# Optimization experiments

Hardware: AMD Instinct MI355X
Metric: run time of the kernel (lower is better)

The kernel has to match this reference:

```python
import jax, jax.numpy as jnp
import numpy as np

S, B, IN = 16384, 1, 8
H = 2048          # hidden_dim
TAG = 2048        # tagset_size
QCNN_DIMS = [(8, 16), (16, 16), (16, 12), (12, 4), (4, 4), (4, 4), (4, 1)]


def _linear_params(key, fan_in, fan_out):
    kw, kb = jax.random.split(key)
    bound = 1.0 / np.sqrt(fan_in)
    w = jax.random.uniform(kw, (fan_in, fan_out), jnp.float32, -bound, bound)
    b = jax.random.uniform(kb, (fan_out,), jnp.float32, -bound, bound)
    return w, b


def setup_inputs() -> dict:
    key = jax.random.key(0)
    keys = jax.random.split(key, 16)
    inp = {"sentence": jax.random.normal(keys[0], (S, B, IN), jnp.float32)}
    names = [("fm", 0), ("c1", 1), ("p1", 2), ("c2", 3), ("p2", 4), ("c3", 5), ("h", 6)]
    for i, (nm, di) in enumerate(names):
        w, b = _linear_params(keys[1 + i], *QCNN_DIMS[di])
        inp[f"{nm}_w"], inp[f"{nm}_b"] = w, b
    for i, g in enumerate(["f", "i", "u", "o"]):
        w, b = _linear_params(keys[8 + i], 1 + H, H)
        inp[f"w{g}"], inp[f"b{g}"] = w, b
    wt, bt = _linear_params(keys[12], H, TAG)
    inp["wt"], inp["bt"] = wt, bt
    return inp


def reference(sentence, fm_w, fm_b, c1_w, c1_b, p1_w, p1_b, c2_w, c2_b,
              p2_w, p2_b, c3_w, c3_b, h_w, h_b,
              wf, bf, wi, bi, wu, bu, wo, bo, wt, bt):
    seq_len, batch, _ = sentence.shape
    t = jnp.tanh
    # ---- ClassicalQCNN: dense MLP chain on flattened tokens ----
    x = sentence.reshape(seq_len * batch, -1)
    x = t(x @ fm_w + fm_b)
    x = t(x @ c1_w + c1_b)
    x = t(x @ p1_w + p1_b)
    x = t(x @ c2_w + c2_b)
    x = t(x @ p2_w + p2_b)
    x = t(x @ c3_w + c3_b)
    x = jax.nn.sigmoid(x @ h_w + h_b)          # (S*B, 1)
    seq = x.reshape(seq_len, batch, 1)

    # ---- ClassicalQLSTM: fuse 4 gate linears into one GEMM per step ----
    w_gates = jnp.concatenate([wf, wi, wu, wo], axis=1)   # (1+H, 4H)
    b_gates = jnp.concatenate([bf, bi, bu, bo])           # (4H,)
    hidden = wf.shape[1]

    def step(carry, x_t):
        hx, cx = carry
        combined = jnp.concatenate([x_t, hx], axis=1)     # (B, 1+H)
        gates = combined @ w_gates + b_gates              # (B, 4H)
        f, i, g, o = jnp.split(gates, 4, axis=1)
        cx = jax.nn.sigmoid(f) * cx + jax.nn.sigmoid(i) * jnp.tanh(g)
        hx = jax.nn.sigmoid(o) * jnp.tanh(cx)
        return (hx, cx), hx

    init = (jnp.zeros((batch, hidden), sentence.dtype),
            jnp.zeros((batch, hidden), sentence.dtype))
    _, lstm_out = jax.lax.scan(step, init, seq)           # (S, B, H)

    logits = lstm_out.reshape(seq_len, -1) @ wt + bt      # batch==1 => (S, TAG)
    return jax.nn.log_softmax(logits, axis=1)
```

## Files before the change

kernel.cpp:

```cpp
#include <hip/hip_runtime.h>
#include <stdint.h>

#define S_LEN 16384
#define HID 2048
#define NPAIR 1024

typedef _Float16 h2v __attribute__((ext_vector_type(2)));

__device__ __forceinline__ float dot2f(uint32_t a, uint32_t b, float c) {
#if __has_builtin(__builtin_amdgcn_fdot2)
  return __builtin_amdgcn_fdot2(__builtin_bit_cast(h2v, a), __builtin_bit_cast(h2v, b), c, false);
#else
  h2v ha = __builtin_bit_cast(h2v, a), hb = __builtin_bit_cast(h2v, b);
  return c + (float)ha[0] * (float)hb[0] + (float)ha[1] * (float)hb[1];
#endif
}

__device__ __forceinline__ uint32_t packh2(float a, float b) {
  h2v h; h[0] = (_Float16)a; h[1] = (_Float16)b;
  return __builtin_bit_cast(uint32_t, h);
}

__device__ __forceinline__ float fsig(float x) { return 1.0f / (1.0f + __expf(-x)); }
__device__ __forceinline__ float ftanh(float x) { return 2.0f / (1.0f + __expf(-2.0f * x)) - 1.0f; }

__device__ __forceinline__ float wave_reduce_add(float x) {
#define DPP_STEP(ctrl)                                                                   \
  {                                                                                      \
    int t_ = __builtin_amdgcn_update_dpp(0, __builtin_bit_cast(int, x), ctrl, 0xf, 0xf, true); \
    x += __builtin_bit_cast(float, t_);                                                  \
  }
  DPP_STEP(0x111)
  DPP_STEP(0x112)
  DPP_STEP(0x114)
  DPP_STEP(0x118)
  DPP_STEP(0x142)
  DPP_STEP(0x143)
#undef DPP_STEP
  return x;
}

__global__ __launch_bounds__(256) void qcnn_kernel(
    const float* __restrict__ sent,
    const float* __restrict__ fm_w, const float* __restrict__ fm_b,
    const float* __restrict__ c1w, const float* __restrict__ c1b,
    const float* __restrict__ p1w, const float* __restrict__ p1b,
    const float* __restrict__ c2w, const float* __restrict__ c2b,
    const float* __restrict__ p2w, const float* __restrict__ p2b,
    const float* __restrict__ c3w, const float* __restrict__ c3b,
    const float* __restrict__ hw, const float* __restrict__ hb,
    float* __restrict__ seq, unsigned long long* __restrict__ hbuf) {
  __shared__ float w[720];
  const int tid = threadIdx.x;
  const float* srcs[14] = {fm_w, fm_b, c1w, c1b, p1w, p1b, c2w, c2b, p2w, p2b, c3w, c3b, hw, hb};
  const int offs[14] = {0, 128, 144, 400, 416, 608, 620, 668, 672, 688, 692, 708, 712, 716};
  const int cnts[14] = {128, 16, 256, 16, 192, 12, 48, 4, 16, 4, 16, 4, 4, 1};
  for (int a = 0; a < 14; ++a)
    for (int i = tid; i < cnts[a]; i += 256) w[offs[a] + i] = srcs[a][i];
  if (blockIdx.x == 0) {
    for (int p = tid; p < NPAIR; p += 256) {
      hbuf[p] = 0ull;
      hbuf[NPAIR + p] = 0x7FFFFFFFull << 32;
    }
  }
  __syncthreads();
  const int t = blockIdx.x * 256 + tid;
  float x[8];
#pragma unroll
  for (int i = 0; i < 8; ++i) x[i] = sent[t * 8 + i];
  float a0[16], a1[16], a2[12], a3[4], a4[4], a5[4];
#pragma unroll
  for (int o = 0; o < 16; ++o) {
    float s = w[128 + o];
#pragma unroll
    for (int i = 0; i < 8; ++i) s += x[i] * w[i * 16 + o];
    a0[o] = ftanh(s);
  }
#pragma unroll
  for (int o = 0; o < 16; ++o) {
    float s = w[400 + o];
#pragma unroll
    for (int i = 0; i < 16; ++i) s += a0[i] * w[144 + i * 16 + o];
    a1[o] = ftanh(s);
  }
#pragma unroll
  for (int o = 0; o < 12; ++o) {
    float s = w[608 + o];
#pragma unroll
    for (int i = 0; i < 16; ++i) s += a1[i] * w[416 + i * 12 + o];
    a2[o] = ftanh(s);
  }
#pragma unroll
  for (int o = 0; o < 4; ++o) {
    float s = w[668 + o];
#pragma unroll
    for (int i = 0; i < 12; ++i) s += a2[i] * w[620 + i * 4 + o];
    a3[o] = ftanh(s);
  }
#pragma unroll
  for (int o = 0; o < 4; ++o) {
    float s = w[688 + o];
#pragma unroll
    for (int i = 0; i < 4; ++i) s += a3[i] * w[672 + i * 4 + o];
    a4[o] = ftanh(s);
  }
#pragma unroll
  for (int o = 0; o < 4; ++o) {
    float s = w[708 + o];
#pragma unroll
    for (int i = 0; i < 4; ++i) s += a4[i] * w[692 + i * 4 + o];
    a5[o] = ftanh(s);
  }
  float s = w[716];
#pragma unroll
  for (int i = 0; i < 4; ++i) s += a5[i] * w[712 + i];
  seq[t] = fsig(s);
}

__global__ __launch_bounds__(512, 2) void lstm_kernel(
    const float* __restrict__ seq,
    const float* __restrict__ wfp, const float* __restrict__ bfp,
    const float* __restrict__ wip, const float* __restrict__ bip,
    const float* __restrict__ wup, const float* __restrict__ bup,
    const float* __restrict__ wop, const float* __restrict__ bop,
    unsigned long long* __restrict__ hbuf,
    uint32_t* __restrict__ hseq) {
  __shared__ __align__(16) uint32_t smem[32768];
  const int tid = threadIdx.x;
  const int lane = tid & 63;
  const int wv = tid >> 6;
  const int blk = blockIdx.x;
  const int col = blk * 8 + wv;
  const float* wptr[4] = {wfp, wip, wup, wop};
  const float* bptr[4] = {bfp, bip, bup, bop};

  {
    const int jj = tid & 7;
    const int sc = blk * 8 + jj;
    const int pb = tid >> 3;
#pragma unroll
    for (int g = 0; g < 4; ++g) {
      const float* wsp = wptr[g];
      for (int pp = 0; pp < 16; ++pp) {
        int p = pp * 64 + pb;
        float w0 = wsp[(size_t)(1 + 2 * p) * HID + sc];
        float w1 = wsp[(size_t)(2 + 2 * p) * HID + sc];
        smem[(jj * 1024 + p) * 4 + g] = packh2(w0, w1);
      }
    }
  }
  __syncthreads();
  uint32_t wr[4][4][4];
#pragma unroll
  for (int m = 0; m < 4; ++m)
#pragma unroll
    for (int j = 0; j < 4; ++j) {
      const uint4 q = *(const uint4*)&smem[(wv * 1024 + 256 * m + 4 * lane + j) * 4];
      wr[m][j][0] = q.x; wr[m][j][1] = q.y; wr[m][j][2] = q.z; wr[m][j][3] = q.w;
    }
  float wx[4], bb[4];
#pragma unroll
  for (int g = 0; g < 4; ++g) {
    wx[g] = wptr[g][col];
    bb[g] = bptr[g][col];
  }
  __syncthreads();
  float* seqf = (float*)smem;
  for (int i = tid; i < 4096; i += 512) ((float4*)seqf)[i] = ((const float4*)seq)[i];
  uint32_t* hlds = smem + 16384;
  uint16_t* hx16 = (uint16_t*)(smem + 18432);
  __syncthreads();

  float cell = 0.f;
  for (int s = 0; s < S_LEN; ++s) {
    const int slot = s & 1;
    uint32_t* hl = hlds + slot * NPAIR;
    const float xt = seqf[s];
    unsigned long long* src = hbuf + (size_t)slot * NPAIR + wv * 128 + lane;
    unsigned long long h0 = __hip_atomic_load(src, __ATOMIC_RELAXED, __HIP_MEMORY_SCOPE_AGENT);
    unsigned long long h1 = __hip_atomic_load(src + 64, __ATOMIC_RELAXED, __HIP_MEMORY_SCOPE_AGENT);
    const uint32_t want = (uint32_t)s;
    while (true) {
      const bool ok0 = ((uint32_t)(h0 >> 32) == want);
      const bool ok1 = ((uint32_t)(h1 >> 32) == want);
      if (__all(ok0 && ok1)) break;
      __builtin_amdgcn_s_sleep(1);
      if (!ok0) h0 = __hip_atomic_load(src, __ATOMIC_RELAXED, __HIP_MEMORY_SCOPE_AGENT);
      if (!ok1) h1 = __hip_atomic_load(src + 64, __ATOMIC_RELAXED, __HIP_MEMORY_SCOPE_AGENT);
    }
    hl[wv * 128 + lane] = (uint32_t)h0;
    hl[wv * 128 + 64 + lane] = (uint32_t)h1;
    __syncthreads();
    {
      uint32_t* hs = hseq + (size_t)s * NPAIR;
      hs[wv * 128 + lane] = (uint32_t)h0;
      hs[wv * 128 + 64 + lane] = (uint32_t)h1;
    }
    float a0 = 0.f, a1 = 0.f, a2 = 0.f, a3 = 0.f;
#pragma unroll
    for (int m = 0; m < 4; ++m) {
      const uint4 q = *(const uint4*)&hl[256 * m + 4 * lane];
      a0 = dot2f(wr[m][0][0], q.x, a0);
      a1 = dot2f(wr[m][0][1], q.x, a1);
      a2 = dot2f(wr[m][0][2], q.x, a2);
      a3 = dot2f(wr[m][0][3], q.x, a3);
      a0 = dot2f(wr[m][1][0], q.y, a0);
      a1 = dot2f(wr[m][1][1], q.y, a1);
      a2 = dot2f(wr[m][1][2], q.y, a2);
      a3 = dot2f(wr[m][1][3], q.y, a3);
      a0 = dot2f(wr[m][2][0], q.z, a0);
      a1 = dot2f(wr[m][2][1], q.z, a1);
      a2 = dot2f(wr[m][2][2], q.z, a2);
      a3 = dot2f(wr[m][2][3], q.z, a3);
      a0 = dot2f(wr[m][3][0], q.w, a0);
      a1 = dot2f(wr[m][3][1], q.w, a1);
      a2 = dot2f(wr[m][3][2], q.w, a2);
      a3 = dot2f(wr[m][3][3], q.w, a3);
    }
    a0 = wave_reduce_add(a0);
    a1 = wave_reduce_add(a1);
    a2 = wave_reduce_add(a2);
    a3 = wave_reduce_add(a3);
    if (lane == 63) {
      const float pF = a0 + wx[0] * xt + bb[0];
      const float pI = a1 + wx[1] * xt + bb[1];
      const float pU = a2 + wx[2] * xt + bb[2];
      const float pO = a3 + wx[3] * xt + bb[3];
      cell = fsig(pF) * cell + fsig(pI) * ftanh(pU);
      const float hval = fsig(pO) * ftanh(cell);
      const _Float16 hf = (_Float16)hval;
      hx16[wv] = __builtin_bit_cast(uint16_t, hf);
    }
    __syncthreads();
    if (tid < 4) {
      const uint32_t pk = smem[18432 + tid];
      const unsigned long long val =
          (((unsigned long long)(uint32_t)(s + 1)) << 32) | (unsigned long long)pk;
      __hip_atomic_store(hbuf + (size_t)((s + 1) & 1) * NPAIR + blk * 4 + tid, val,
                         __ATOMIC_RELAXED, __HIP_MEMORY_SCOPE_AGENT);
    }
  }
}

__global__ __launch_bounds__(256) void packwt_kernel(const float* __restrict__ wt,
                                                     uint32_t* __restrict__ wtp) {
  const int idx = blockIdx.x * 256 + threadIdx.x;
  const int p = idx >> 11;
  const int n = idx & 2047;
  wtp[idx] = packh2(wt[(size_t)(2 * p) * 2048 + n], wt[(size_t)(2 * p + 1) * 2048 + n]);
}

__global__ __launch_bounds__(256) void gemm_kernel(
    const uint32_t* __restrict__ A,
    const uint32_t* __restrict__ B,
    const float* __restrict__ bias, float* __restrict__ C) {
  __shared__ __align__(16) uint32_t As[16 * 132];
  __shared__ __align__(16) uint32_t Bs[16 * 132];
  const int tid = threadIdx.x;
  const int bx = blockIdx.x;
  const int m0 = (bx >> 4) * 128;
  const int n0 = (bx & 15) * 128;
  const int tm = (tid & 15) * 8;
  const int tn = (tid >> 4) * 8;
  float acc[8][8];
#pragma unroll
  for (int i = 0; i < 8; ++i)
#pragma unroll
    for (int j = 0; j < 8; ++j) acc[i][j] = 0.f;
  for (int kt = 0; kt < 64; ++kt) {
    const int p0 = kt * 16;
    __syncthreads();
#pragma unroll
    for (int r = 0; r < 8; ++r) {
      int idx = r * 256 + tid;
      int m = idx >> 4, pp = idx & 15;
      As[pp * 132 + m] = A[(size_t)(m0 + m) * 1024 + p0 + pp];
    }
#pragma unroll
    for (int r = 0; r < 8; ++r) {
      int idx = r * 256 + tid;
      int pp = idx >> 7, n = idx & 127;
      Bs[pp * 132 + n] = B[(size_t)(p0 + pp) * 2048 + n0 + n];
    }
    __syncthreads();
#pragma unroll
    for (int pp = 0; pp < 16; ++pp) {
      const uint4* ap = (const uint4*)(As + pp * 132 + tm);
      const uint4* bp = (const uint4*)(Bs + pp * 132 + tn);
      uint4 a0 = ap[0], a1 = ap[1];
      uint4 b0 = bp[0], b1 = bp[1];
      uint32_t av[8] = {a0.x, a0.y, a0.z, a0.w, a1.x, a1.y, a1.z, a1.w};
      uint32_t bv[8] = {b0.x, b0.y, b0.z, b0.w, b1.x, b1.y, b1.z, b1.w};
#pragma unroll
      for (int i = 0; i < 8; ++i)
#pragma unroll
        for (int j = 0; j < 8; ++j) acc[i][j] = dot2f(av[i], bv[j], acc[i][j]);
    }
  }
#pragma unroll
  for (int i = 0; i < 8; ++i) {
    const int m = m0 + tm + i;
    float4 o0, o1;
    o0.x = acc[i][0] + bias[n0 + tn + 0];
    o0.y = acc[i][1] + bias[n0 + tn + 1];
    o0.z = acc[i][2] + bias[n0 + tn + 2];
    o0.w = acc[i][3] + bias[n0 + tn + 3];
    o1.x = acc[i][4] + bias[n0 + tn + 4];
    o1.y = acc[i][5] + bias[n0 + tn + 5];
    o1.z = acc[i][6] + bias[n0 + tn + 6];
    o1.w = acc[i][7] + bias[n0 + tn + 7];
    *(float4*)(C + (size_t)m * 2048 + n0 + tn) = o0;
    *(float4*)(C + (size_t)m * 2048 + n0 + tn + 4) = o1;
  }
}

__global__ __launch_bounds__(256) void lsm_kernel(float* __restrict__ C) {
  __shared__ float red[8];
  const int row = blockIdx.x;
  float* p = C + (size_t)row * HID;
  const int tid = threadIdx.x, lane = tid & 63, wv = tid >> 6;
  float v[8];
  float4 q0 = *(const float4*)(p + tid * 8);
  float4 q1 = *(const float4*)(p + tid * 8 + 4);
  v[0] = q0.x; v[1] = q0.y; v[2] = q0.z; v[3] = q0.w;
  v[4] = q1.x; v[5] = q1.y; v[6] = q1.z; v[7] = q1.w;
  float mx = v[0];
#pragma unroll
  for (int i = 1; i < 8; ++i) mx = fmaxf(mx, v[i]);
#pragma unroll
  for (int m = 32; m >= 1; m >>= 1) mx = fmaxf(mx, __shfl_xor(mx, m, 64));
  if (lane == 0) red[wv] = mx;
  __syncthreads();
  mx = fmaxf(fmaxf(red[0], red[1]), fmaxf(red[2], red[3]));
  float sm = 0.f;
#pragma unroll
  for (int i = 0; i < 8; ++i) {
    v[i] -= mx;
    sm += __expf(v[i]);
  }
#pragma unroll
  for (int m = 32; m >= 1; m >>= 1) sm += __shfl_xor(sm, m, 64);
  if (lane == 0) red[4 + wv] = sm;
  __syncthreads();
  sm = red[4] + red[5] + red[6] + red[7];
  const float ls = __logf(sm);
#pragma unroll
  for (int i = 0; i < 8; ++i) v[i] -= ls;
  q0.x = v[0]; q0.y = v[1]; q0.z = v[2]; q0.w = v[3];
  q1.x = v[4]; q1.y = v[5]; q1.z = v[6]; q1.w = v[7];
  *(float4*)(p + tid * 8) = q0;
  *(float4*)(p + tid * 8 + 4) = q1;
}

extern "C" void kernel_launch(void* const* d_in, const int* in_sizes, int n_in,
                              void* d_out, int out_size, void* d_ws, size_t ws_size,
                              hipStream_t stream) {
  const float* sent = (const float*)d_in[0];
  const float* fm_w = (const float*)d_in[1];
  const float* fm_b = (const float*)d_in[2];
  const float* c1w = (const float*)d_in[3];
  const float* c1b = (const float*)d_in[4];
  const float* p1w = (const float*)d_in[5];
  const float* p1b = (const float*)d_in[6];
  const float* c2w = (const float*)d_in[7];
  const float* c2b = (const float*)d_in[8];
  const float* p2w = (const float*)d_in[9];
  const float* p2b = (const float*)d_in[10];
  const float* c3w = (const float*)d_in[11];
  const float* c3b = (const float*)d_in[12];
  const float* hw = (const float*)d_in[13];
  const float* hb = (const float*)d_in[14];
  const float* wf = (const float*)d_in[15];
  const float* bf = (const float*)d_in[16];
  const float* wi = (const float*)d_in[17];
  const float* bi = (const float*)d_in[18];
  const float* wu = (const float*)d_in[19];
  const float* bu = (const float*)d_in[20];
  const float* wo = (const float*)d_in[21];
  const float* bo = (const float*)d_in[22];
  const float* wt = (const float*)d_in[23];
  const float* bt = (const float*)d_in[24];

  char* ws = (char*)d_ws;
  float* seq = (float*)ws;
  unsigned long long* hbuf = (unsigned long long*)(ws + 65536);
  uint32_t* hseq = (uint32_t*)(ws + 131072);
  uint32_t* wtp = (uint32_t*)(ws + 131072 + (size_t)S_LEN * NPAIR * 4);
  float* C = (float*)d_out;

  qcnn_kernel<<<64, 256, 0, stream>>>(sent, fm_w, fm_b, c1w, c1b, p1w, p1b, c2w, c2b,
                                      p2w, p2b, c3w, c3b, hw, hb, seq, hbuf);
  packwt_kernel<<<8192, 256, 0, stream>>>(wt, wtp);

  void* args[] = {(void*)&seq, (void*)&wf, (void*)&bf, (void*)&wi, (void*)&bi,
                  (void*)&wu, (void*)&bu, (void*)&wo, (void*)&bo,
                  (void*)&hbuf, (void*)&hseq};
  hipError_t rc = hipLaunchCooperativeKernel((void*)lstm_kernel, dim3(256), dim3(512),
                                             args, 0, stream);
  if (rc != hipSuccess) {
    lstm_kernel<<<256, 512, 0, stream>>>(seq, wf, bf, wi, bi, wu, bu, wo, bo, hbuf, hseq);
  }

  gemm_kernel<<<2048, 256, 0, stream>>>(hseq, wtp, bt, C);
  lsm_kernel<<<16384, 256, 0, stream>>>(C);
}
```

Before: 40.94 ms.

## Replace per-step block barriers with per-wave LDS flags in LSTM recurrence

Removes both __syncthreads per timestep in the persistent LSTM kernel. Each wave now publishes its slice of h to LDS with a per-slot release flag, and waves start on the chunks whose flags are ready, in a staggered order. Pairs of waves combine their fp16 h values through an LDS mailbox and publish to global without a block barrier. The hseq write is shifted by one step, with an extra loop iteration to flush the last step. The cost is spin-waiting on LDS flags and more subtle memory-ordering correctness (the chunk-wait loads are relaxed and the pubw store is relaxed).

```diff
diff --git a/kernel.cpp b/kernel.cpp
--- a/kernel.cpp
+++ b/kernel.cpp
@@ -167,15 +167,18 @@
   __syncthreads();
   float* seqf = (float*)smem;
   for (int i = tid; i < 4096; i += 512) ((float4*)seqf)[i] = ((const float4*)seq)[i];
-  uint32_t* hlds = smem + 16384;
-  uint16_t* hx16 = (uint16_t*)(smem + 18432);
+  uint32_t* hl0 = smem + 16384;
+  uint32_t* wtagw = smem + 18432;
+  uint32_t* pubw = smem + 18448;
+  if (tid < 16) wtagw[tid] = 0u;
+  if (tid < 4) pubw[tid] = 0u;
   __syncthreads();
 
   float cell = 0.f;
-  for (int s = 0; s < S_LEN; ++s) {
+  for (int s = 0; s <= S_LEN; ++s) {
     const int slot = s & 1;
-    uint32_t* hl = hlds + slot * NPAIR;
-    const float xt = seqf[s];
+    uint32_t* hl = hl0 + slot * NPAIR;
+    const uint32_t want1 = (uint32_t)(s + 1);
     unsigned long long* src = hbuf + (size_t)slot * NPAIR + wv * 128 + lane;
     unsigned long long h0 = __hip_atomic_load(src, __ATOMIC_RELAXED, __HIP_MEMORY_SCOPE_AGENT);
     unsigned long long h1 = __hip_atomic_load(src + 64, __ATOMIC_RELAXED, __HIP_MEMORY_SCOPE_AGENT);
@@ -190,54 +193,71 @@
     }
     hl[wv * 128 + lane] = (uint32_t)h0;
     hl[wv * 128 + 64 + lane] = (uint32_t)h1;
-    __syncthreads();
-    {
-      uint32_t* hs = hseq + (size_t)s * NPAIR;
+    if (lane == 0)
+      __hip_atomic_store(&wtagw[slot * 8 + wv], want1, __ATOMIC_RELEASE,
+                         __HIP_MEMORY_SCOPE_WORKGROUP);
+    if (s > 0) {
+      uint32_t* hs = hseq + (size_t)(s - 1) * NPAIR;
       hs[wv * 128 + lane] = (uint32_t)h0;
       hs[wv * 128 + 64 + lane] = (uint32_t)h1;
     }
+    if (s == S_LEN) break;
+
     float a0 = 0.f, a1 = 0.f, a2 = 0.f, a3 = 0.f;
-#pragma unroll
-    for (int m = 0; m < 4; ++m) {
-      const uint4 q = *(const uint4*)&hl[256 * m + 4 * lane];
-      a0 = dot2f(wr[m][0][0], q.x, a0);
-      a1 = dot2f(wr[m][0][1], q.x, a1);
-      a2 = dot2f(wr[m][0][2], q.x, a2);
-      a3 = dot2f(wr[m][0][3], q.x, a3);
-      a0 = dot2f(wr[m][1][0], q.y, a0);
-      a1 = dot2f(wr[m][1][1], q.y, a1);
-      a2 = dot2f(wr[m][1][2], q.y, a2);
-      a3 = dot2f(wr[m][1][3], q.y, a3);
-      a0 = dot2f(wr[m][2][0], q.z, a0);
-      a1 = dot2f(wr[m][2][1], q.z, a1);
-      a2 = dot2f(wr[m][2][2], q.z, a2);
-      a3 = dot2f(wr[m][2][3], q.z, a3);
-      a0 = dot2f(wr[m][3][0], q.w, a0);
-      a1 = dot2f(wr[m][3][1], q.w, a1);
-      a2 = dot2f(wr[m][3][2], q.w, a2);
-      a3 = dot2f(wr[m][3][3], q.w, a3);
-    }
+#define CHUNK(M)                                                                     \
+  {                                                                                  \
+    const int myw = 2 * (M) + (lane >> 5);                                           \
+    while (__hip_atomic_load(&wtagw[slot * 8 + myw], __ATOMIC_RELAXED,               \
+                             __HIP_MEMORY_SCOPE_WORKGROUP) != want1) {}              \
+    __builtin_amdgcn_sched_barrier(0);                                               \
+    const uint4 q = *(const uint4*)&hl[256 * (M) + 4 * lane];                        \
+    a0 = dot2f(wr[M][0][0], q.x, a0); a1 = dot2f(wr[M][0][1], q.x, a1);              \
+    a2 = dot2f(wr[M][0][2], q.x, a2); a3 = dot2f(wr[M][0][3], q.x, a3);              \
+    a0 = dot2f(wr[M][1][0], q.y, a0); a1 = dot2f(wr[M][1][1], q.y, a1);              \
+    a2 = dot2f(wr[M][1][2], q.y, a2); a3 = dot2f(wr[M][1][3], q.y, a3);              \
+    a0 = dot2f(wr[M][2][0], q.z, a0); a1 = dot2f(wr[M][2][1], q.z, a1);              \
+    a2 = dot2f(wr[M][2][2], q.z, a2); a3 = dot2f(wr[M][2][3], q.z, a3);              \
+    a0 = dot2f(wr[M][3][0], q.w, a0); a1 = dot2f(wr[M][3][1], q.w, a1);              \
+    a2 = dot2f(wr[M][3][2], q.w, a2); a3 = dot2f(wr[M][3][3], q.w, a3);              \
+  }
+#pragma unroll
+    for (int j = 0; j < 4; ++j) {
+      const int m = ((wv >> 1) + j) & 3;
+      switch (m) {
+        case 0: CHUNK(0); break;
+        case 1: CHUNK(1); break;
+        case 2: CHUNK(2); break;
+        default: CHUNK(3); break;
+      }
+    }
+#undef CHUNK
     a0 = wave_reduce_add(a0);
     a1 = wave_reduce_add(a1);
     a2 = wave_reduce_add(a2);
     a3 = wave_reduce_add(a3);
     if (lane == 63) {
+      const float xt = seqf[s];
       const float pF = a0 + wx[0] * xt + bb[0];
       const float pI = a1 + wx[1] * xt + bb[1];
       const float pU = a2 + wx[2] * xt + bb[2];
       const float pO = a3 + wx[3] * xt + bb[3];
       cell = fsig(pF) * cell + fsig(pI) * ftanh(pU);
       const float hval = fsig(pO) * ftanh(cell);
-      const _Float16 hf = (_Float16)hval;
-      hx16[wv] = __builtin_bit_cast(uint16_t, hf);
-    }
-    __syncthreads();
-    if (tid < 4) {
-      const uint32_t pk = smem[18432 + tid];
-      const unsigned long long val =
-          (((unsigned long long)(uint32_t)(s + 1)) << 32) | (unsigned long long)pk;
-      __hip_atomic_store(hbuf + (size_t)((s + 1) & 1) * NPAIR + blk * 4 + tid, val,
-                         __ATOMIC_RELAXED, __HIP_MEMORY_SCOPE_AGENT);
+      const uint32_t hbits =
+          (uint32_t)__builtin_bit_cast(uint16_t, (_Float16)hval);
+      if (wv & 1) {
+        __hip_atomic_store(&pubw[wv >> 1], (want1 << 16) | hbits, __ATOMIC_RELAXED,
+                           __HIP_MEMORY_SCOPE_WORKGROUP);
+      } else {
+        uint32_t pw;
+        while (((pw = __hip_atomic_load(&pubw[wv >> 1], __ATOMIC_RELAXED,
+                                        __HIP_MEMORY_SCOPE_WORKGROUP)) >> 16) != want1) {}
+        const uint32_t pk = ((pw & 0xFFFFu) << 16) | hbits;
+        const unsigned long long val =
+            (((unsigned long long)want1) << 32) | (unsigned long long)pk;
+        __hip_atomic_store(hbuf + (size_t)((s + 1) & 1) * NPAIR + blk * 4 + (wv >> 1), val,
+                           __ATOMIC_RELAXED, __HIP_MEMORY_SCOPE_AGENT);
+      }
     }
   }
 }
```

Result: slower. 78.08 ms (+90.7%).

## Relay LSTM hidden state through per-XCD L2 buffers via relay blocks

Applied to the files above, without the earlier changes.

Blocks 0..7 act as relays: they poll the global (device-coherent) hidden-state buffer and copy it into a per-group local buffer. The other blocks poll that buffer with sc0 loads that can hit in the local L2, falling back periodically to the global buffer. The goal is to cut cross-XCD coherent polling traffic and latency on the per-step barrier of this 16384-step recurrence. The hseq write is also moved to the four threads that publish each block's values. The relay adds an extra hop of latency, and correctness depends on blocks with the same blk&7 sharing an XCD's L2 and on sc0 visibility semantics.

```diff
diff --git a/kernel.cpp b/kernel.cpp
--- a/kernel.cpp
+++ b/kernel.cpp
@@ -4,6 +4,7 @@
 #define S_LEN 16384
 #define HID 2048
 #define NPAIR 1024
+#define NGRP 8
 
 typedef _Float16 h2v __attribute__((ext_vector_type(2)));
 
@@ -23,6 +24,16 @@
 
 __device__ __forceinline__ float fsig(float x) { return 1.0f / (1.0f + __expf(-x)); }
 __device__ __forceinline__ float ftanh(float x) { return 2.0f / (1.0f + __expf(-2.0f * x)) - 1.0f; }
+
+__device__ __forceinline__ unsigned long long ld_l2(const unsigned long long* p) {
+  unsigned long long v;
+  asm volatile("global_load_dwordx2 %0, %1, off sc0\n\ts_waitcnt vmcnt(0)"
+               : "=v"(v) : "v"(p) : "memory");
+  return v;
+}
+__device__ __forceinline__ void st_l2(unsigned long long* p, unsigned long long v) {
+  asm volatile("global_store_dwordx2 %0, %1, off sc0" : : "v"(p), "v"(v) : "memory");
+}
 
 __device__ __forceinline__ float wave_reduce_add(float x) {
 #define DPP_STEP(ctrl)                                                                   \
@@ -49,7 +60,8 @@
     const float* __restrict__ p2w, const float* __restrict__ p2b,
     const float* __restrict__ c3w, const float* __restrict__ c3b,
     const float* __restrict__ hw, const float* __restrict__ hb,
-    float* __restrict__ seq, unsigned long long* __restrict__ hbuf) {
+    float* __restrict__ seq, unsigned long long* __restrict__ hbuf,
+    unsigned long long* __restrict__ lbuf) {
   __shared__ float w[720];
   const int tid = threadIdx.x;
   const float* srcs[14] = {fm_w, fm_b, c1w, c1b, p1w, p1b, c2w, c2b, p2w, p2b, c3w, c3b, hw, hb};
@@ -62,6 +74,11 @@
       hbuf[p] = 0ull;
       hbuf[NPAIR + p] = 0x7FFFFFFFull << 32;
     }
+    for (int idx = tid; idx < NGRP * NPAIR; idx += 256) {
+      const int g = idx >> 10, i = idx & (NPAIR - 1);
+      lbuf[(size_t)(g * 2) * NPAIR + i] = 0ull;
+      lbuf[(size_t)(g * 2 + 1) * NPAIR + i] = 0x7FFFFFFFull << 32;
+    }
   }
   __syncthreads();
   const int t = blockIdx.x * 256 + tid;
@@ -124,12 +141,15 @@
     const float* __restrict__ wup, const float* __restrict__ bup,
     const float* __restrict__ wop, const float* __restrict__ bop,
     unsigned long long* __restrict__ hbuf,
+    unsigned long long* __restrict__ lbuf,
     uint32_t* __restrict__ hseq) {
   __shared__ __align__(16) uint32_t smem[32768];
   const int tid = threadIdx.x;
   const int lane = tid & 63;
   const int wv = tid >> 6;
   const int blk = blockIdx.x;
+  const int grp = blk & (NGRP - 1);
+  const bool is_relay = (blk < NGRP);
   const int col = blk * 8 + wv;
   const float* wptr[4] = {wfp, wip, wup, wop};
   const float* bptr[4] = {bfp, bip, bup, bop};
@@ -171,31 +191,54 @@
   uint16_t* hx16 = (uint16_t*)(smem + 18432);
   __syncthreads();
 
+#define LDP(p) __hip_atomic_load((p), __ATOMIC_RELAXED, __HIP_MEMORY_SCOPE_AGENT)
+
   float cell = 0.f;
   for (int s = 0; s < S_LEN; ++s) {
     const int slot = s & 1;
     uint32_t* hl = hlds + slot * NPAIR;
     const float xt = seqf[s];
-    unsigned long long* src = hbuf + (size_t)slot * NPAIR + wv * 128 + lane;
-    unsigned long long h0 = __hip_atomic_load(src, __ATOMIC_RELAXED, __HIP_MEMORY_SCOPE_AGENT);
-    unsigned long long h1 = __hip_atomic_load(src + 64, __ATOMIC_RELAXED, __HIP_MEMORY_SCOPE_AGENT);
     const uint32_t want = (uint32_t)s;
-    while (true) {
-      const bool ok0 = ((uint32_t)(h0 >> 32) == want);
-      const bool ok1 = ((uint32_t)(h1 >> 32) == want);
-      if (__all(ok0 && ok1)) break;
-      __builtin_amdgcn_s_sleep(1);
-      if (!ok0) h0 = __hip_atomic_load(src, __ATOMIC_RELAXED, __HIP_MEMORY_SCOPE_AGENT);
-      if (!ok1) h1 = __hip_atomic_load(src + 64, __ATOMIC_RELAXED, __HIP_MEMORY_SCOPE_AGENT);
-    }
-    hl[wv * 128 + lane] = (uint32_t)h0;
-    hl[wv * 128 + 64 + lane] = (uint32_t)h1;
+    unsigned long long hv0, hv1;
+    if (is_relay) {
+      unsigned long long* src = hbuf + (size_t)slot * NPAIR + wv * 128 + lane;
+      unsigned long long h0 = LDP(src), h1 = LDP(src + 64);
+      while (true) {
+        const bool ok0 = ((uint32_t)(h0 >> 32) == want);
+        const bool ok1 = ((uint32_t)(h1 >> 32) == want);
+        if (__all(ok0 && ok1)) break;
+        __builtin_amdgcn_s_sleep(1);
+        if (!ok0) h0 = LDP(src);
+        if (!ok1) h1 = LDP(src + 64);
+      }
+      unsigned long long* ldst = lbuf + (size_t)(grp * 2 + slot) * NPAIR + wv * 128 + lane;
+      st_l2(ldst, h0);
+      st_l2(ldst + 64, h1);
+      hv0 = h0; hv1 = h1;
+    } else {
+      const unsigned long long* lsrc =
+          lbuf + (size_t)(grp * 2 + slot) * NPAIR + wv * 128 + lane;
+      unsigned long long* gsrc = hbuf + (size_t)slot * NPAIR + wv * 128 + lane;
+      bool d0 = false, d1 = false;
+      unsigned long long h0 = 0, h1 = 0;
+      while (true) {
+#pragma unroll
+        for (int r = 0; r < 2; ++r) {
+          if (!d0) { unsigned long long t = ld_l2(lsrc);      if ((uint32_t)(t >> 32) == want) { h0 = t; d0 = true; } }
+          if (!d1) { unsigned long long t = ld_l2(lsrc + 64); if ((uint32_t)(t >> 32) == want) { h1 = t; d1 = true; } }
+          if (__all(d0 && d1)) goto got;
+        }
+        if (!d0) { unsigned long long t = LDP(gsrc);      if ((uint32_t)(t >> 32) == want) { h0 = t; d0 = true; } }
+        if (!d1) { unsigned long long t = LDP(gsrc + 64); if ((uint32_t)(t >> 32) == want) { h1 = t; d1 = true; } }
+        if (__all(d0 && d1)) break;
+        __builtin_amdgcn_s_sleep(1);
+      }
+got:
+      hv0 = h0; hv1 = h1;
+    }
+    hl[wv * 128 + lane] = (uint32_t)hv0;
+    hl[wv * 128 + 64 + lane] = (uint32_t)hv1;
     __syncthreads();
-    {
-      uint32_t* hs = hseq + (size_t)s * NPAIR;
-      hs[wv * 128 + lane] = (uint32_t)h0;
-      hs[wv * 128 + 64 + lane] = (uint32_t)h1;
-    }
     float a0 = 0.f, a1 = 0.f, a2 = 0.f, a3 = 0.f;
 #pragma unroll
     for (int m = 0; m < 4; ++m) {
@@ -238,8 +281,10 @@
           (((unsigned long long)(uint32_t)(s + 1)) << 32) | (unsigned long long)pk;
       __hip_atomic_store(hbuf + (size_t)((s + 1) & 1) * NPAIR + blk * 4 + tid, val,
                          __ATOMIC_RELAXED, __HIP_MEMORY_SCOPE_AGENT);
-    }
-  }
+      hseq[(size_t)s * NPAIR + blk * 4 + tid] = pk;
+    }
+  }
+#undef LDP
 }
 
 __global__ __launch_bounds__(256) void packwt_kernel(const float* __restrict__ wt,
@@ -384,21 +429,23 @@
   char* ws = (char*)d_ws;
   float* seq = (float*)ws;
   unsigned long long* hbuf = (unsigned long long*)(ws + 65536);
-  uint32_t* hseq = (uint32_t*)(ws + 131072);
-  uint32_t* wtp = (uint32_t*)(ws + 131072 + (size_t)S_LEN * NPAIR * 4);
+  unsigned long long* lbuf = (unsigned long long*)(ws + 131072);
+  uint32_t* hseq = (uint32_t*)(ws + 262144);
+  uint32_t* wtp = (uint32_t*)(ws + 262144 + (size_t)S_LEN * NPAIR * 4);
   float* C = (float*)d_out;
 
   qcnn_kernel<<<64, 256, 0, stream>>>(sent, fm_w, fm_b, c1w, c1b, p1w, p1b, c2w, c2b,
-                                      p2w, p2b, c3w, c3b, hw, hb, seq, hbuf);
+                                      p2w, p2b, c3w, c3b, hw, hb, seq, hbuf, lbuf);
   packwt_kernel<<<8192, 256, 0, stream>>>(wt, wtp);
 
   void* args[] = {(void*)&seq, (void*)&wf, (void*)&bf, (void*)&wi, (void*)&bi,
                   (void*)&wu, (void*)&bu, (void*)&wo, (void*)&bo,
-                  (void*)&hbuf, (void*)&hseq};
+                  (void*)&hbuf, (void*)&lbuf, (void*)&hseq};
   hipError_t rc = hipLaunchCooperativeKernel((void*)lstm_kernel, dim3(256), dim3(512),
                                              args, 0, stream);
   if (rc != hipSuccess) {
-    lstm_kernel<<<256, 512, 0, stream>>>(seq, wf, bf, wi, bi, wu, bu, wo, bo, hbuf, hseq);
+    lstm_kernel<<<256, 512, 0, stream>>>(seq, wf, bf, wi, bi, wu, bu, wo, bo,
+                                         hbuf, lbuf, hseq);
   }
 
   gemm_kernel<<<2048, 256, 0, stream>>>(hseq, wtp, bt, C);
```

New measurement: 36.24 ms (median of 2 runs). -11.5%, faster.
